# Kernel optimization log

Hardware: AMD Instinct MI355X
Metric: run time of the kernel (lower is better)

## Reference

```python
import jax, jax.numpy as jnp
import numpy as np

N = 4096
IN = 64          # input_size
QD = 16          # query_vector_dim
CI = 2 * IN + 1  # 129, MLP_Param input dim


def _xavier(key, shape):
    fan_in, fan_out = shape[-2], shape[-1]
    bound = float(np.sqrt(6.0 / (fan_in + fan_out)))
    return jax.random.uniform(key, shape, jnp.float32, -bound, bound)


def setup_inputs() -> dict:
    key = jax.random.key(0)
    ks = jax.random.split(key, 10)
    return {
        "x": jax.random.normal(ks[0], (N, IN + 1), jnp.float32),
        "h": jax.random.normal(ks[1], (N, IN), jnp.float32),
        "query_vectors": jax.random.normal(ks[2], (N, QD), jnp.float32),
        "adj": jax.random.uniform(ks[3], (N, N), jnp.float32),
        "nodes_ind": jnp.arange(N, dtype=jnp.int64 if jax.config.jax_enable_x64 else jnp.int32),
        "W_r": _xavier(ks[4], (QD, CI, IN)),
        "b_r": _xavier(ks[5], (QD, IN)),
        "W_u": _xavier(ks[6], (QD, CI, IN)),
        "b_u": _xavier(ks[7], (QD, IN)),
        "W_c": _xavier(ks[8], (QD, CI, IN)),
        "b_c": _xavier(ks[9], (QD, IN)),
    }


def _mlp_param(xv, q, W, b):
    # per-node dynamic weights: [n, CI, IN]
    Wn = jnp.einsum('nd,dio->nio', q, W)
    return jnp.einsum('ni,nio->no', xv, Wn) + q @ b


def reference(x, h, query_vectors, adj, nodes_ind, W_r, b_r, W_u, b_u, W_c, b_c):
    combined = adj @ jnp.concatenate([x, h], axis=-1)          # [N, 129]
    cg = combined[nodes_ind]                                    # [M, 129]
    r = jax.nn.sigmoid(_mlp_param(cg, query_vectors, W_r, b_r))
    u = jax.nn.sigmoid(_mlp_param(cg, query_vectors, W_u, b_u))
    h2 = h.at[nodes_ind].set(r * h[nodes_ind])                  # h[nodes_ind] = r*h[nodes_ind]
    combined_new = jnp.concatenate([x, h2], axis=-1)[nodes_ind]  # no adj mixing second time
    cand = jnp.tanh(_mlp_param(combined_new, query_vectors, W_c, b_c))
    return (1.0 - u) * h2[nodes_ind] + u * cand
```

## Files before the change

kernel.cpp:

```cpp
#include <hip/hip_runtime.h>
#include <math.h>


#define NN   4096
#define XCC  65
#define HCC  64
#define QDIM 16
#define CI   129
#define CST  132
#define AKST 520
#define GSTRIDE 147456

typedef unsigned short u16;
typedef __attribute__((ext_vector_type(4))) unsigned short ushort4_t;
typedef __attribute__((ext_vector_type(8))) unsigned short ushort8_t;
typedef __attribute__((ext_vector_type(8))) short bf16x8;
typedef __attribute__((ext_vector_type(16))) float f32x16;

__device__ __forceinline__ void split2(float a, u16& hi, u16& lo) {
  unsigned u = __float_as_uint(a);
  hi = (u16)(u >> 16);
  float rec = __uint_as_float(u & 0xFFFF0000u);
  float lf = a - rec;
  unsigned v = __float_as_uint(lf);
  v += 0x7FFF + ((v >> 16) & 1);
  lo = (u16)(v >> 16);
}

__device__ __forceinline__ void gload_lds16(const void* gsrc, void* ldst) {
  __builtin_amdgcn_global_load_lds(
      (const __attribute__((address_space(1))) unsigned int*)gsrc,
      (__attribute__((address_space(3))) unsigned int*)ldst, 16, 0, 0);
}

__global__ __launch_bounds__(256) void k0_pack(const float* __restrict__ x,
                                               const float* __restrict__ h,
                                               u16* __restrict__ Bh,
                                               u16* __restrict__ Bl,
                                               const float* __restrict__ Wr,
                                               const float* __restrict__ Wu,
                                               const float* __restrict__ Wc,
                                               u16* __restrict__ Wh,
                                               u16* __restrict__ Wl) {
  __shared__ float sT[64][161];
  const int t = threadIdx.x;
  if (blockIdx.x < 64) {
    const int n0 = blockIdx.x * 64;
    for (int f = t; f < 64 * XCC; f += 256) {
      int n = f / XCC, c = f - n * XCC;
      sT[n][c] = x[(size_t)(n0 + n) * XCC + c];
    }
    for (int f = t; f < 64 * HCC; f += 256) {
      int n = f >> 6, c = f & 63;
      sT[n][XCC + c] = h[(size_t)(n0 + n) * HCC + c];
    }
    for (int f = t; f < 64 * 31; f += 256) {
      int n = f / 31, c = f - n * 31;
      sT[n][CI + c] = 0.f;
    }
    __syncthreads();
    for (int idx = t; idx < 5 * 4 * 64; idx += 256) {
      const int lane = idx & 63;
      const int ksl = (idx >> 6) & 3;
      const int ct = idx >> 8;
      const int nl = ksl * 16 + (lane >> 5) * 8;
      const int feat = ct * 32 + (lane & 31);
      ushort8_t vh, vl;
#pragma unroll
      for (int j = 0; j < 8; ++j) {
        u16 hi, lo; split2(sT[nl + j][feat], hi, lo);
        vh[j] = hi; vl[j] = lo;
      }
      const size_t off = (((size_t)ct * 256 + (blockIdx.x * 4) + ksl) * 64 + lane) * 8;
      *(ushort8_t*)(Bh + off) = vh;
      *(ushort8_t*)(Bl + off) = vl;
    }
  } else {
    int gid = (blockIdx.x - 64) * 256 + t;
    if (gid >= 3 * 16 * 2 * 9 * 64) return;
    int lane = gid & 63;
    int rest = gid >> 6;
    int kst = rest % 9; rest /= 9;
    int ct = rest & 1; rest >>= 1;
    int d = rest & 15; rest >>= 4;
    const float* W = (rest == 0) ? Wr : (rest == 1 ? Wu : Wc);
    const int o = ct * 32 + (lane & 31);
    const int i0 = kst * 16 + (lane >> 5) * 8;
    ushort8_t vh, vl;
#pragma unroll
    for (int j = 0; j < 8; ++j) {
      int i = i0 + j;
      float v = (i < CI) ? W[((size_t)d * CI + i) * 64 + o] : 0.f;
      u16 hi, lo; split2(v, hi, lo);
      vh[j] = hi; vl[j] = lo;
    }
    const size_t off = (size_t)gid * 8;
    *(ushort8_t*)(Wh + off) = vh;
    *(ushort8_t*)(Wl + off) = vl;
  }
}

template <int SPK>
__global__ __launch_bounds__(256, 4) void k1_mfma(const float* __restrict__ adj,
                                                  const u16* __restrict__ Bh,
                                                  const u16* __restrict__ Bl,
                                                  float* __restrict__ P1) {
  constexpr int KLEN = 4096 / SPK;
  constexpr int STEPS = KLEN / 16;
  __shared__ u16 sAh[2][2][64][8];
  __shared__ u16 sAl[2][2][64][8];
  __shared__ u16 sB[3][10][512];
  __shared__ u16 sScratch[512];
  const int t = threadIdx.x;
  const int lane = t & 63;
  const int w = t >> 6;
  const int rgrp = w & 1;
  const int cthalf = w >> 1;
  const int m0 = blockIdx.x * 64;
  const int sp = blockIdx.y;
  const int ct0 = cthalf ? 3 : 0;
  const int R = t >> 2;
  const int ksts = t & 3;
  const int srg = R >> 5, srl = R & 31;
  const int skh = ksts >> 1, sj0 = (ksts & 1) * 4;

  f32x16 a0, a1, a2;
#pragma unroll
  for (int r = 0; r < 16; ++r) { a0[r] = 0.f; a1[r] = 0.f; a2[r] = 0.f; }

  const float* aptr = adj + (size_t)(m0 + R) * NN + sp * KLEN + ksts * 4;
  float4 va, vb, vc;

#define LOADA(it, tgt) tgt = *(const float4*)(aptr + (it) * 16);

#define CONV4(src, abuf)                                                       \
  {                                                                            \
    u16 h0, h1, h2, h3, l0, l1, l2, l3;                                        \
    split2(src.x, h0, l0); split2(src.y, h1, l1);                              \
    split2(src.z, h2, l2); split2(src.w, h3, l3);                              \
    ushort4_t hv = {h0, h1, h2, h3};                                           \
    ushort4_t lv = {l0, l1, l2, l3};                                           \
    *(ushort4_t*)&sAh[abuf][srg][srl + 32 * skh][sj0] = hv;                    \
    *(ushort4_t*)&sAl[abuf][srg][srl + 32 * skh][sj0] = lv;                    \
  }

#define BDMA(it, bbuf)                                                         \
  {                                                                            \
    _Pragma("unroll")                                                          \
    for (int j = 0; j < 3; ++j) {                                              \
      const int c = w + 4 * j;                                                 \
      const int ct = (c < 10) ? (c >> 1) : 0;                                  \
      const int hl = (c < 10) ? (c & 1) : 0;                                   \
      const int ks = sp * STEPS + (it);                                        \
      const u16* src =                                                         \
          (hl ? Bl : Bh) + (((size_t)ct * 256 + ks) * 64 + lane) * 8;          \
      gload_lds16(src, (c < 10) ? &sB[bbuf][c][0] : &sScratch[0]);             \
    }                                                                          \
  }

#define BAR(N)                                                                 \
  asm volatile("s_waitcnt vmcnt(" #N ") lgkmcnt(0)" ::: "memory");             \
  __builtin_amdgcn_sched_barrier(0);                                           \
  __builtin_amdgcn_s_barrier();                                                \
  __builtin_amdgcn_sched_barrier(0);

#define COMPUTE(abuf, bbuf)                                                    \
  {                                                                            \
    bf16x8 ah = *(const bf16x8*)&sAh[abuf][rgrp][lane][0];                     \
    bf16x8 al = *(const bf16x8*)&sAl[abuf][rgrp][lane][0];                     \
    const int cb = ct0 * 2;                                                    \
    bf16x8 b0h = *(const bf16x8*)&sB[bbuf][cb + 0][lane * 8];                  \
    bf16x8 b0l = *(const bf16x8*)&sB[bbuf][cb + 1][lane * 8];                  \
    bf16x8 b1h = *(const bf16x8*)&sB[bbuf][cb + 2][lane * 8];                  \
    bf16x8 b1l = *(const bf16x8*)&sB[bbuf][cb + 3][lane * 8];                  \
    a0 = __builtin_amdgcn_mfma_f32_32x32x16_bf16(ah, b0h, a0, 0, 0, 0);        \
    a1 = __builtin_amdgcn_mfma_f32_32x32x16_bf16(ah, b1h, a1, 0, 0, 0);        \
    a0 = __builtin_amdgcn_mfma_f32_32x32x16_bf16(al, b0h, a0, 0, 0, 0);        \
    a1 = __builtin_amdgcn_mfma_f32_32x32x16_bf16(al, b1h, a1, 0, 0, 0);        \
    a0 = __builtin_amdgcn_mfma_f32_32x32x16_bf16(ah, b0l, a0, 0, 0, 0);        \
    a1 = __builtin_amdgcn_mfma_f32_32x32x16_bf16(ah, b1l, a1, 0, 0, 0);        \
    if (cthalf == 0) {                                                         \
      bf16x8 b2h = *(const bf16x8*)&sB[bbuf][cb + 4][lane * 8];                \
      bf16x8 b2l = *(const bf16x8*)&sB[bbuf][cb + 5][lane * 8];                \
      a2 = __builtin_amdgcn_mfma_f32_32x32x16_bf16(ah, b2h, a2, 0, 0, 0);      \
      a2 = __builtin_amdgcn_mfma_f32_32x32x16_bf16(al, b2h, a2, 0, 0, 0);      \
      a2 = __builtin_amdgcn_mfma_f32_32x32x16_bf16(ah, b2l, a2, 0, 0, 0);      \
    }                                                                          \
  }

  LOADA(0, va);
  BDMA(0, 0);
  LOADA(1, vb);
  BDMA(1, 1);
  LOADA(2, vc);
  CONV4(va, 0);
  BAR(5)
#pragma unroll
  for (int it = 0; it < STEPS; ++it) {
    const int abuf = it & 1;
    const int bbuf = it % 3;
    if (it < STEPS - 2) BDMA(it + 2, (it + 2) % 3);
    if (it <= STEPS - 4) {
      if ((it % 3) == 0) { LOADA(it + 3, va); }
      else if ((it % 3) == 1) { LOADA(it + 3, vb); }
      else { LOADA(it + 3, vc); }
    }
    COMPUTE(abuf, bbuf);
    if (it < STEPS - 1) {
      if (((it + 1) % 3) == 0) { CONV4(va, abuf ^ 1); }
      else if (((it + 1) % 3) == 1) { CONV4(vb, abuf ^ 1); }
      else { CONV4(vc, abuf ^ 1); }
    }
    if (it <= STEPS - 4) { BAR(5) }
    else if (it == STEPS - 3) { BAR(4) }
    else if (it == STEPS - 2) { BAR(0) }
  }
#undef LOADA
#undef CONV4
#undef BDMA
#undef BAR
#undef COMPUTE
  float* outp = P1 + (size_t)sp * NN * CST;
  const int colb = lane & 31;
  const int rbase = m0 + rgrp * 32 + 4 * (lane >> 5);
  {
    const int colg = ct0 * 32 + colb;
#pragma unroll
    for (int r = 0; r < 16; ++r)
      outp[(size_t)(rbase + (r & 3) + 8 * (r >> 2)) * CST + colg] = a0[r];
  }
  {
    const int colg = (ct0 + 1) * 32 + colb;
    if (colg < CST) {
#pragma unroll
      for (int r = 0; r < 16; ++r)
        outp[(size_t)(rbase + (r & 3) + 8 * (r >> 2)) * CST + colg] = a1[r];
    }
  }
  if (cthalf == 0) {
    const int colg = 64 + colb;
#pragma unroll
    for (int r = 0; r < 16; ++r)
      outp[(size_t)(rbase + (r & 3) + 8 * (r >> 2)) * CST + colg] = a2[r];
  }
}


#define PACKA()                                                                \
  for (int s = t; s < 9 * 64; s += 512) {                                      \
    int kst = s >> 6, l = s & 63;                                              \
    int row = l & 31, k0i = kst * 16 + (l >> 5) * 8;                           \
    ushort8_t vh, vl;                                                          \
    _Pragma("unroll")                                                          \
    for (int j = 0; j < 8; ++j) {                                              \
      u16 hi, lo; split2(sXV[row][k0i + j], hi, lo);                           \
      vh[j] = hi; vl[j] = lo;                                                  \
    }                                                                          \
    *(ushort8_t*)&sAh[kst * AKST + l * 8] = vh;                                \
    *(ushort8_t*)&sAl[kst * AKST + l * 8] = vl;                                \
  }

template <int SPK>
__global__ __launch_bounds__(512) void k23_fused(
    const float* __restrict__ P1, const float* __restrict__ x,
    const float* __restrict__ h, const float* __restrict__ q,
    const u16* __restrict__ Wh, const u16* __restrict__ Wl,
    const float* __restrict__ br, const float* __restrict__ bu,
    const float* __restrict__ bc, float* __restrict__ out) {
  __shared__ float sXV[32][144];
  __shared__ u16 sAh[9 * AKST], sAl[9 * AKST];
  __shared__ float sQ[32][16];
  __shared__ float sXfer[8][16][64];
  const int t = threadIdx.x;
  const int n0 = blockIdx.x * 32;
  const int cto = blockIdx.y;
  for (int f = t; f < 32 * 33; f += 512) {
    int n = f / 33, c4 = f - n * 33;
    const float* p = P1 + (size_t)(n0 + n) * CST + c4 * 4;
    float sx = 0.f, sy = 0.f, sz = 0.f, sw = 0.f;
#pragma unroll
    for (int sp = 0; sp < SPK; ++sp) {
      float4 v = *(const float4*)(p + (size_t)sp * NN * CST);
      sx += v.x; sy += v.y; sz += v.z; sw += v.w;
    }
    sXV[n][c4 * 4 + 0] = sx; sXV[n][c4 * 4 + 1] = sy;
    sXV[n][c4 * 4 + 2] = sz; sXV[n][c4 * 4 + 3] = sw;
  }
  for (int f = t; f < 32 * 3; f += 512) {
    float4 z = {0, 0, 0, 0};
    *(float4*)&sXV[f / 3][132 + (f % 3) * 4] = z;
  }
  sQ[t >> 4][t & 15] = q[(size_t)(n0 + (t >> 4)) * QDIM + (t & 15)];
  __syncthreads();
  PACKA();
  __syncthreads();
  for (int f = t; f < 32 * 65; f += 512) {
    int n = f / 65, i = f - n * 65;
    sXV[n][i] = x[(size_t)(n0 + n) * XCC + i];
  }
  const int lane = t & 63, dh = t >> 6;

  auto mfma_target = [&](const u16* gh, const u16* gl, int ct_sel,
                         float& o0, float& o1) {
    f32x16 acc;
#pragma unroll
    for (int r = 0; r < 16; ++r) acc[r] = 0.f;
#pragma unroll
    for (int dd = 0; dd < 2; ++dd) {
      const int d = dh * 2 + dd;
      const size_t bb = (((size_t)d * 2 + ct_sel) * 9 * 64 + lane) * 8;
      f32x16 t0, t1, t2;
#pragma unroll
      for (int r = 0; r < 16; ++r) { t0[r] = 0.f; t1[r] = 0.f; t2[r] = 0.f; }
#pragma unroll
      for (int kst = 0; kst < 9; ++kst) {
        bf16x8 ah = *(const bf16x8*)&sAh[kst * AKST + lane * 8];
        bf16x8 al = *(const bf16x8*)&sAl[kst * AKST + lane * 8];
        bf16x8 bh = *(const bf16x8*)(gh + bb + kst * 512);
        bf16x8 bl = *(const bf16x8*)(gl + bb + kst * 512);
        t0 = __builtin_amdgcn_mfma_f32_32x32x16_bf16(ah, bh, t0, 0, 0, 0);
        t1 = __builtin_amdgcn_mfma_f32_32x32x16_bf16(al, bh, t1, 0, 0, 0);
        t2 = __builtin_amdgcn_mfma_f32_32x32x16_bf16(ah, bl, t2, 0, 0, 0);
      }
#pragma unroll
      for (int r = 0; r < 16; ++r) {
        int node = (r & 3) + 8 * (r >> 2) + 4 * (lane >> 5);
        acc[r] += sQ[node][d] * (t0[r] + t1[r] + t2[r]);
      }
    }
    __syncthreads();
#pragma unroll
    for (int r = 0; r < 16; ++r) sXfer[dh][r][lane] = acc[r];
    __syncthreads();
    const int rr0 = dh * 2, rr1 = dh * 2 + 1;
    float s0 = 0.f, s1 = 0.f;
#pragma unroll
    for (int wv = 0; wv < 8; ++wv) {
      s0 += sXfer[wv][rr0][lane];
      s1 += sXfer[wv][rr1][lane];
    }
    o0 = s0; o1 = s1;
  };

  auto add_bias = [&](const float* bias, int node, int col, float pre) {
#pragma unroll
    for (int d = 0; d < 16; ++d) pre += sQ[node][d] * bias[(size_t)d * 64 + col];
    return pre;
  };

  float r0p0, r0p1, r1p0, r1p1, up0, up1;
  mfma_target(Wh, Wl, 0, r0p0, r0p1);
  mfma_target(Wh, Wl, 1, r1p0, r1p1);
  mfma_target(Wh + GSTRIDE, Wl + GSTRIDE, cto, up0, up1);

  const int col0 = lane & 31, col1 = 32 + col0, colu = cto * 32 + col0;
  float uval[2], h2own[2];
#pragma unroll
  for (int i = 0; i < 2; ++i) {
    const int rr = dh * 2 + i;
    const int node = (rr & 3) + 8 * (rr >> 2) + 4 * (lane >> 5);
    float pr0 = add_bias(br, node, col0, i ? r0p1 : r0p0);
    float pr1 = add_bias(br, node, col1, i ? r1p1 : r1p0);
    float pu  = add_bias(bu, node, colu, i ? up1 : up0);
    float rg0 = 1.f / (1.f + expf(-pr0));
    float rg1 = 1.f / (1.f + expf(-pr1));
    uval[i] = 1.f / (1.f + expf(-pu));
    float h2a = rg0 * h[(size_t)(n0 + node) * HCC + col0];
    float h2b = rg1 * h[(size_t)(n0 + node) * HCC + col1];
    sXV[node][XCC + col0] = h2a;
    sXV[node][XCC + col1] = h2b;
    h2own[i] = cto ? h2b : h2a;
  }
  __syncthreads();
  PACKA();
  __syncthreads();
  float cp0, cp1;
  mfma_target(Wh + 2 * GSTRIDE, Wl + 2 * GSTRIDE, cto, cp0, cp1);
#pragma unroll
  for (int i = 0; i < 2; ++i) {
    const int rr = dh * 2 + i;
    const int node = (rr & 3) + 8 * (rr >> 2) + 4 * (lane >> 5);
    float pc = add_bias(bc, node, colu, i ? cp1 : cp0);
    float cand = tanhf(pc);
    out[(size_t)(n0 + node) * HCC + colu] =
        (1.f - uval[i]) * h2own[i] + uval[i] * cand;
  }
}

extern "C" void kernel_launch(void* const* d_in, const int* in_sizes, int n_in,
                              void* d_out, int out_size, void* d_ws, size_t ws_size,
                              hipStream_t stream) {
  const float* x   = (const float*)d_in[0];
  const float* h   = (const float*)d_in[1];
  const float* q   = (const float*)d_in[2];
  const float* adj = (const float*)d_in[3];
  const float* Wr  = (const float*)d_in[5];
  const float* br  = (const float*)d_in[6];
  const float* Wu  = (const float*)d_in[7];
  const float* bu  = (const float*)d_in[8];
  const float* Wc  = (const float*)d_in[9];
  const float* bc  = (const float*)d_in[10];
  float* out = (float*)d_out;

  const size_t NEED16 = (size_t)16 * NN * CST * 4 + 2162688 + 10485760 + 1769472;
  const int spk = (ws_size >= NEED16) ? 16 : 8;

  char* ws = (char*)d_ws;
  const size_t OFF_P1 = 0;
  const size_t OFF_XV = OFF_P1 + (size_t)spk * NN * CST * 4;
  const size_t OFF_BP = OFF_XV + (size_t)NN * CST * 4;
  const size_t OFF_WH = OFF_BP + (size_t)2 * 5 * 256 * 64 * 8 * 2;
  const size_t OFF_WL = OFF_WH + (size_t)3 * GSTRIDE * 2;
  float* P1 = (float*)(ws + OFF_P1);
  u16*   Bh = (u16*)(ws + OFF_BP);
  u16*   Bl = (u16*)(ws + OFF_BP + (size_t)5 * 256 * 64 * 8 * 2);
  u16*   Wh = (u16*)(ws + OFF_WH);
  u16*   Wl = (u16*)(ws + OFF_WL);

  hipLaunchKernelGGL(k0_pack, dim3(280), dim3(256), 0, stream,
                     x, h, Bh, Bl, Wr, Wu, Wc, Wh, Wl);
  if (spk == 16) {
    hipLaunchKernelGGL(k1_mfma<16>, dim3(64, 16), dim3(256), 0, stream, adj, Bh, Bl, P1);
    hipLaunchKernelGGL(k23_fused<16>, dim3(128, 2), dim3(512), 0, stream,
                       P1, x, h, q, Wh, Wl, br, bu, bc, out);
  } else {
    hipLaunchKernelGGL(k1_mfma<8>, dim3(64, 8), dim3(256), 0, stream, adj, Bh, Bl, P1);
    hipLaunchKernelGGL(k23_fused<8>, dim3(128, 2), dim3(512), 0, stream,
                       P1, x, h, q, Wh, Wl, br, bu, bc, out);
  }
}
```

Baseline: 67.88 us.

## Fuse r0, r1 and u MFMA passes into one interleaved loop

```diff
diff --git a/kernel.cpp b/kernel.cpp
--- a/kernel.cpp
+++ b/kernel.cpp
@@ -9,6 +9,7 @@
 #define CI   129
 #define CST  132
 #define AKST 520
+#define XVST 148
 #define GSTRIDE 147456
 
 typedef unsigned short u16;
@@ -267,10 +268,12 @@
     const u16* __restrict__ Wh, const u16* __restrict__ Wl,
     const float* __restrict__ br, const float* __restrict__ bu,
     const float* __restrict__ bc, float* __restrict__ out) {
-  __shared__ float sXV[32][144];
+  __shared__ float sXV[32][XVST];
   __shared__ u16 sAh[9 * AKST], sAl[9 * AKST];
   __shared__ float sQ[32][16];
-  __shared__ float sXfer[8][16][64];
+  __shared__ float sX0[8][16][64];
+  __shared__ float sX1[8][16][64];
+  __shared__ float sX2[8][16][64];
   const int t = threadIdx.x;
   const int n0 = blockIdx.x * 32;
   const int cto = blockIdx.y;
@@ -300,15 +303,105 @@
   }
   const int lane = t & 63, dh = t >> 6;
 
-  auto mfma_target = [&](const u16* gh, const u16* gl, int ct_sel,
-                         float& o0, float& o1) {
+  f32x16 aR0, aR1, aU;
+#pragma unroll
+  for (int r = 0; r < 16; ++r) { aR0[r] = 0.f; aR1[r] = 0.f; aU[r] = 0.f; }
+#pragma unroll
+  for (int dd = 0; dd < 2; ++dd) {
+    const int d = dh * 2 + dd;
+    const size_t bR0 = (((size_t)d * 2 + 0) * 9 * 64 + lane) * 8;
+    const size_t bR1 = (((size_t)d * 2 + 1) * 9 * 64 + lane) * 8;
+    const size_t bU  = (((size_t)d * 2 + cto) * 9 * 64 + lane) * 8 + GSTRIDE;
+    f32x16 t0, t1, t2;
+#pragma unroll
+    for (int r = 0; r < 16; ++r) { t0[r] = 0.f; t1[r] = 0.f; t2[r] = 0.f; }
+#pragma unroll
+    for (int kst = 0; kst < 9; ++kst) {
+      bf16x8 ah = *(const bf16x8*)&sAh[kst * AKST + lane * 8];
+      bf16x8 al = *(const bf16x8*)&sAl[kst * AKST + lane * 8];
+      bf16x8 b0h = *(const bf16x8*)(Wh + bR0 + kst * 512);
+      bf16x8 b0l = *(const bf16x8*)(Wl + bR0 + kst * 512);
+      bf16x8 b1h = *(const bf16x8*)(Wh + bR1 + kst * 512);
+      bf16x8 b1l = *(const bf16x8*)(Wl + bR1 + kst * 512);
+      bf16x8 buh = *(const bf16x8*)(Wh + bU + kst * 512);
+      bf16x8 bul = *(const bf16x8*)(Wl + bU + kst * 512);
+      t0 = __builtin_amdgcn_mfma_f32_32x32x16_bf16(ah, b0h, t0, 0, 0, 0);
+      t1 = __builtin_amdgcn_mfma_f32_32x32x16_bf16(ah, b1h, t1, 0, 0, 0);
+      t2 = __builtin_amdgcn_mfma_f32_32x32x16_bf16(ah, buh, t2, 0, 0, 0);
+      t0 = __builtin_amdgcn_mfma_f32_32x32x16_bf16(al, b0h, t0, 0, 0, 0);
+      t1 = __builtin_amdgcn_mfma_f32_32x32x16_bf16(al, b1h, t1, 0, 0, 0);
+      t2 = __builtin_amdgcn_mfma_f32_32x32x16_bf16(al, buh, t2, 0, 0, 0);
+      t0 = __builtin_amdgcn_mfma_f32_32x32x16_bf16(ah, b0l, t0, 0, 0, 0);
+      t1 = __builtin_amdgcn_mfma_f32_32x32x16_bf16(ah, b1l, t1, 0, 0, 0);
+      t2 = __builtin_amdgcn_mfma_f32_32x32x16_bf16(ah, bul, t2, 0, 0, 0);
+    }
+#pragma unroll
+    for (int r = 0; r < 16; ++r) {
+      int node = (r & 3) + 8 * (r >> 2) + 4 * (lane >> 5);
+      float qd = sQ[node][d];
+      aR0[r] += qd * t0[r]; aR1[r] += qd * t1[r]; aU[r] += qd * t2[r];
+    }
+  }
+#pragma unroll
+  for (int r = 0; r < 16; ++r) {
+    sX0[dh][r][lane] = aR0[r];
+    sX1[dh][r][lane] = aR1[r];
+    sX2[dh][r][lane] = aU[r];
+  }
+  __syncthreads();
+
+  auto add_bias = [&](const float* bias, int node, int col, float pre) {
+#pragma unroll
+    for (int d = 0; d < 16; ++d) pre += sQ[node][d] * bias[(size_t)d * 64 + col];
+    return pre;
+  };
+
+  float r0p[2], r1p[2], up[2];
+#pragma unroll
+  for (int i = 0; i < 2; ++i) {
+    const int rr = dh * 2 + i;
+    float a = 0.f, b = 0.f, c = 0.f;
+#pragma unroll
+    for (int wv = 0; wv < 8; ++wv) {
+      a += sX0[wv][rr][lane];
+      b += sX1[wv][rr][lane];
+      c += sX2[wv][rr][lane];
+    }
+    r0p[i] = a; r1p[i] = b; up[i] = c;
+  }
+
+  const int col0 = lane & 31, col1 = 32 + col0, colu = cto * 32 + col0;
+  float uval[2], h2own[2];
+#pragma unroll
+  for (int i = 0; i < 2; ++i) {
+    const int rr = dh * 2 + i;
+    const int node = (rr & 3) + 8 * (rr >> 2) + 4 * (lane >> 5);
+    float pr0 = add_bias(br, node, col0, r0p[i]);
+    float pr1 = add_bias(br, node, col1, r1p[i]);
+    float pu  = add_bias(bu, node, colu, up[i]);
+    float rg0 = 1.f / (1.f + expf(-pr0));
+    float rg1 = 1.f / (1.f + expf(-pr1));
+    uval[i] = 1.f / (1.f + expf(-pu));
+    float h2a = rg0 * h[(size_t)(n0 + node) * HCC + col0];
+    float h2b = rg1 * h[(size_t)(n0 + node) * HCC + col1];
+    sXV[node][XCC + col0] = h2a;
+    sXV[node][XCC + col1] = h2b;
+    h2own[i] = cto ? h2b : h2a;
+  }
+  __syncthreads();
+  PACKA();
+  __syncthreads();
+
+  {
+    const u16* gh = Wh + (size_t)2 * GSTRIDE;
+    const u16* gl = Wl + (size_t)2 * GSTRIDE;
     f32x16 acc;
 #pragma unroll
     for (int r = 0; r < 16; ++r) acc[r] = 0.f;
 #pragma unroll
     for (int dd = 0; dd < 2; ++dd) {
       const int d = dh * 2 + dd;
-      const size_t bb = (((size_t)d * 2 + ct_sel) * 9 * 64 + lane) * 8;
+      const size_t bb = (((size_t)d * 2 + cto) * 9 * 64 + lane) * 8;
       f32x16 t0, t1, t2;
 #pragma unroll
       for (int r = 0; r < 16; ++r) { t0[r] = 0.f; t1[r] = 0.f; t2[r] = 0.f; }
@@ -328,59 +421,18 @@
         acc[r] += sQ[node][d] * (t0[r] + t1[r] + t2[r]);
       }
     }
-    __syncthreads();
-#pragma unroll
-    for (int r = 0; r < 16; ++r) sXfer[dh][r][lane] = acc[r];
-    __syncthreads();
-    const int rr0 = dh * 2, rr1 = dh * 2 + 1;
-    float s0 = 0.f, s1 = 0.f;
-#pragma unroll
-    for (int wv = 0; wv < 8; ++wv) {
-      s0 += sXfer[wv][rr0][lane];
-      s1 += sXfer[wv][rr1][lane];
-    }
-    o0 = s0; o1 = s1;
-  };
-
-  auto add_bias = [&](const float* bias, int node, int col, float pre) {
-#pragma unroll
-    for (int d = 0; d < 16; ++d) pre += sQ[node][d] * bias[(size_t)d * 64 + col];
-    return pre;
-  };
-
-  float r0p0, r0p1, r1p0, r1p1, up0, up1;
-  mfma_target(Wh, Wl, 0, r0p0, r0p1);
-  mfma_target(Wh, Wl, 1, r1p0, r1p1);
-  mfma_target(Wh + GSTRIDE, Wl + GSTRIDE, cto, up0, up1);
-
-  const int col0 = lane & 31, col1 = 32 + col0, colu = cto * 32 + col0;
-  float uval[2], h2own[2];
+#pragma unroll
+    for (int r = 0; r < 16; ++r) sX0[dh][r][lane] = acc[r];
+  }
+  __syncthreads();
 #pragma unroll
   for (int i = 0; i < 2; ++i) {
     const int rr = dh * 2 + i;
     const int node = (rr & 3) + 8 * (rr >> 2) + 4 * (lane >> 5);
-    float pr0 = add_bias(br, node, col0, i ? r0p1 : r0p0);
-    float pr1 = add_bias(br, node, col1, i ? r1p1 : r1p0);
-    float pu  = add_bias(bu, node, colu, i ? up1 : up0);
-    float rg0 = 1.f / (1.f + expf(-pr0));
-    float rg1 = 1.f / (1.f + expf(-pr1));
-    uval[i] = 1.f / (1.f + expf(-pu));
-    float h2a = rg0 * h[(size_t)(n0 + node) * HCC + col0];
-    float h2b = rg1 * h[(size_t)(n0 + node) * HCC + col1];
-    sXV[node][XCC + col0] = h2a;
-    sXV[node][XCC + col1] = h2b;
-    h2own[i] = cto ? h2b : h2a;
-  }
-  __syncthreads();
-  PACKA();
-  __syncthreads();
-  float cp0, cp1;
-  mfma_target(Wh + 2 * GSTRIDE, Wl + 2 * GSTRIDE, cto, cp0, cp1);
-#pragma unroll
-  for (int i = 0; i < 2; ++i) {
-    const int rr = dh * 2 + i;
-    const int node = (rr & 3) + 8 * (rr >> 2) + 4 * (lane >> 5);
-    float pc = add_bias(bc, node, colu, i ? cp1 : cp0);
+    float s = 0.f;
+#pragma unroll
+    for (int wv = 0; wv < 8; ++wv) s += sX0[wv][rr][lane];
+    float pc = add_bias(bc, node, colu, s);
     float cand = tanhf(pc);
     out[(size_t)(n0 + node) * HCC + colu] =
         (1.f - uval[i]) * h2own[i] + uval[i] * cand;
```

After: 64.43 us. -5.1%, faster.
